# Kernel optimization log

Measured on AMD Instinct MI355X. Metric: run time of the kernel, lower is better.

The kernel has to match this reference:

```python
import jax, jax.numpy as jnp
import numpy as np

B, S, T, V, E, H, D, A = 16, 128, 128, 32000, 512, 512, 512, 512
ENC = 2 * H  # bidirectional encoder output dim
NEG = -1e9


def _w(key, shape, scale=0.05):
    return scale * jax.random.normal(key, shape, dtype=jnp.float32)


def setup_inputs() -> dict:
    key = jax.random.key(0)
    ks = jax.random.split(key, 26)
    src = jax.random.randint(ks[0], (B, S), 1, V)
    tgt = jax.random.randint(ks[1], (B, T), 1, V)
    src_lens = jnp.full((B,), S, dtype=jnp.int32)  # full-length sequences (pack == identity)
    return dict(
        src=src, src_lens=src_lens, tgt=tgt,
        enc_embed=_w(ks[2], (V, E)).at[0].set(0.0),   # padding_idx=0
        Wih_f=_w(ks[3], (4 * H, E)), Whh_f=_w(ks[4], (4 * H, H)),
        bih_f=_w(ks[5], (4 * H,)), bhh_f=_w(ks[6], (4 * H,)),
        Wih_b=_w(ks[7], (4 * H, E)), Whh_b=_w(ks[8], (4 * H, H)),
        bih_b=_w(ks[9], (4 * H,)), bhh_b=_w(ks[10], (4 * H,)),
        Wbh=_w(ks[11], (D, 2 * H)), bbh=_w(ks[12], (D,)),
        Wbc=_w(ks[13], (D, 2 * H)), bbc=_w(ks[14], (D,)),
        Wh_att=_w(ks[15], (A, ENC)), Ws_att=_w(ks[16], (A, D)), v_att=_w(ks[17], (A,)),
        dec_embed=_w(ks[18], (V, E)).at[0].set(0.0),  # padding_idx=0
        Wih_d=_w(ks[19], (4 * D, E + ENC)), Whh_d=_w(ks[20], (4 * D, D)),
        bih_d=_w(ks[21], (4 * D,)), bhh_d=_w(ks[22], (4 * D,)),
        Wfc=_w(ks[23], (V, D + ENC)), bfc=_w(ks[24], (V,)),
    )


def _lstm_cell(x, h, c, Wih, Whh, bih, bhh):
    # PyTorch gate order: i, f, g, o
    g = x @ Wih.T + h @ Whh.T + (bih + bhh)
    i, f, gg, o = jnp.split(g, 4, axis=-1)
    c = jax.nn.sigmoid(f) * c + jax.nn.sigmoid(i) * jnp.tanh(gg)
    h = jax.nn.sigmoid(o) * jnp.tanh(c)
    return h, c


def _run_lstm(xs, Wih, Whh, bih, bhh, hdim):
    # xs: [S, B, E] -> (hs [S, B, hdim], h_last, c_last)
    b = xs.shape[1]
    h0 = jnp.zeros((b, hdim), xs.dtype)

    def step(carry, x):
        h, c = carry
        h, c = _lstm_cell(x, h, c, Wih, Whh, bih, bhh)
        return (h, c), h

    (hT, cT), hs = jax.lax.scan(step, (h0, h0), xs)
    return hs, hT, cT


def reference(src, src_lens, tgt, enc_embed, Wih_f, Whh_f, bih_f, bhh_f,
              Wih_b, Whh_b, bih_b, bhh_b, Wbh, bbh, Wbc, bbc,
              Wh_att, Ws_att, v_att, dec_embed, Wih_d, Whh_d, bih_d, bhh_d,
              Wfc, bfc):
    # ---- BiLSTM encoder (src_lens == S, so packing is the identity) ----
    emb = enc_embed[src]                      # [B, S, E]
    xs = jnp.swapaxes(emb, 0, 1)              # [S, B, E]
    hs_f, hf, _ = _run_lstm(xs, Wih_f, Whh_f, bih_f, bhh_f, H)
    hs_b, hb, _ = _run_lstm(xs[::-1], Wih_b, Whh_b, bih_b, bhh_b, H)
    hs_b = hs_b[::-1]
    enc_out = jnp.swapaxes(jnp.concatenate([hs_f, hs_b], axis=-1), 0, 1)  # [B, S, 2H]

    # ---- bridge (num_layers = 1) ----
    h_cat = jnp.concatenate([hf, hb], axis=-1)  # [B, 2H]
    h0 = jnp.tanh(h_cat @ Wbh.T + bbh)          # [B, D]
    c_cat = jnp.concatenate([hf, hb], axis=-1)
    c0 = jnp.tanh(c_cat @ Wbc.T + bbc)

    mask = jnp.arange(S)[None, :] < src_lens[:, None]  # [B, S]
    enc_proj = jnp.einsum('bse,ae->bsa', enc_out, Wh_att)  # W_h(enc_out), hoisted

    # ---- decoder loop, teacher_forcing = 1.0 ----
    def dec_step(carry, inp_t):
        h, c = carry
        # Bahdanau attention on top-layer hidden state
        score = jnp.einsum('bsa,a->bs', jnp.tanh(enc_proj + (h @ Ws_att.T)[:, None, :]), v_att)
        score = jnp.where(mask, score, NEG)
        attn = jax.nn.softmax(score, axis=-1)
        ctx = jnp.einsum('bs,bse->be', attn, enc_out)       # [B, 2H]
        x = jnp.concatenate([dec_embed[inp_t], ctx], axis=-1)  # [B, E+2H]
        h, c = _lstm_cell(x, h, c, Wih_d, Whh_d, bih_d, bhh_d)
        logits = jnp.concatenate([h, ctx], axis=-1) @ Wfc.T + bfc  # [B, V]
        return (h, c), logits

    inps = tgt[:, :-1].T  # [T-1, B]
    _, logits = jax.lax.scan(dec_step, (h0, c0), inps)
    return jnp.swapaxes(logits, 0, 1)  # [B, T-1, V]
```

## Files before the change

### kernel.cpp

```cpp
#include <hip/hip_runtime.h>

typedef __bf16 bf16x8 __attribute__((ext_vector_type(8)));
typedef float f32x4 __attribute__((ext_vector_type(4)));
typedef unsigned short us;
typedef unsigned long long ull;

#define DEV static __device__ __forceinline__

DEV float bf2f(us u){ union { unsigned u; float f; } x; x.u = ((unsigned)u) << 16; return x.f; }
DEV us f2bf(float f){
  union { float f; unsigned u; } x; x.f = f;
  unsigned r = x.u + 0x7fffu + ((x.u >> 16) & 1u);
  return (us)(r >> 16);
}
DEV unsigned pack2(us lo, us hi){ return (unsigned)lo | ((unsigned)hi << 16); }
DEV float sigm(float x){ return 1.0f / (1.0f + expf(-x)); }
DEV float tanh_fast(float x){ float e = __expf(2.0f * x); return 1.0f - 2.0f / (e + 1.0f); }
DEV void unpk2(unsigned u, float& a, float& b){ a = bf2f((us)u); b = bf2f((us)(u >> 16)); }

DEV unsigned ld4v(const unsigned* p){ return __hip_atomic_load(p, __ATOMIC_RELAXED, __HIP_MEMORY_SCOPE_AGENT); }
DEV ull ld8v(const void* p){ return __hip_atomic_load((const ull*)p, __ATOMIC_RELAXED, __HIP_MEMORY_SCOPE_AGENT); }
DEV void st4v(unsigned* p, unsigned v){ __hip_atomic_store(p, v, __ATOMIC_RELAXED, __HIP_MEMORY_SCOPE_AGENT); }

DEV void gridbar3(unsigned* arr, unsigned ep){
  __syncthreads();
  if (threadIdx.x == 0)
    __hip_atomic_store(arr + (size_t)blockIdx.x * 16, ep, __ATOMIC_RELEASE, __HIP_MEMORY_SCOPE_AGENT);
  if (threadIdx.x < 128){
    while (__hip_atomic_load(arr + (size_t)threadIdx.x * 16, __ATOMIC_RELAXED, __HIP_MEMORY_SCOPE_AGENT) < ep)
      __builtin_amdgcn_s_sleep(4);
  }
  __syncthreads();
}

__global__ void k_f2bf(const float4* __restrict__ in, uint2* __restrict__ out, long n4){
  long stride = (long)gridDim.x * blockDim.x;
  for (long i = (long)blockIdx.x * blockDim.x + threadIdx.x; i < n4; i += stride){
    float4 v = in[i];
    uint2 o; o.x = pack2(f2bf(v.x), f2bf(v.y)); o.y = pack2(f2bf(v.z), f2bf(v.w));
    out[i] = o;
  }
}

__global__ void k_bias3(const float* a0, const float* b0, float* o0,
                        const float* a1, const float* b1, float* o1,
                        const float* a2, const float* b2, float* o2){
  int i = blockIdx.x * 256 + threadIdx.x;
  o0[i] = a0[i] + b0[i];
  o1[i] = a1[i] + b1[i];
  o2[i] = a2[i] + b2[i];
}

__global__ void k_embed(const int* __restrict__ tok, const float* __restrict__ table,
                        us* __restrict__ out){
  int r = blockIdx.x;
  int b = r & 15, pos = r >> 4;
  int idx = tok[b * 128 + pos];
  float4 v = ((const float4*)(table + (size_t)idx * 512))[threadIdx.x];
  uint2 o; o.x = pack2(f2bf(v.x), f2bf(v.y)); o.y = pack2(f2bf(v.z), f2bf(v.w));
  ((uint2*)(out + (size_t)r * 512))[threadIdx.x] = o;
}

template<int MODE>
__global__ __launch_bounds__(256)
void gemm_bt(const us* __restrict__ A, int lda,
             const us* __restrict__ B, int ldb,
             const float* __restrict__ bias,
             void* __restrict__ Cv, int ldc, int K, int mvalid)
{
  __shared__ __align__(16) us As[128 * 64];
  __shared__ __align__(16) us Bs[128 * 64];
  const int tid  = threadIdx.x;
  const int lane = tid & 63, wid = tid >> 6;
  const int wm = (wid >> 1) * 64, wn = (wid & 1) * 64;
  const us* Ab = A + (size_t)blockIdx.y * 128 * lda;
  const us* Bb = B + (size_t)blockIdx.x * 128 * ldb;

  f32x4 acc[4][4] = {};
  bf16x8 ga[4], gb[4];

  #pragma unroll
  for (int r = 0; r < 4; r++){
    int c = tid + r * 256;
    ga[r] = *(const bf16x8*)(Ab + (size_t)(c >> 3) * lda + (c & 7) * 8);
    gb[r] = *(const bf16x8*)(Bb + (size_t)(c >> 3) * ldb + (c & 7) * 8);
  }
  const int nt = K >> 6;
  for (int t = 0; t < nt; t++){
    #pragma unroll
    for (int r = 0; r < 4; r++){
      int c = tid + r * 256;
      int slot = ((c >> 3) * 8 + ((c & 7) ^ ((c >> 3) & 7))) * 8;
      *(bf16x8*)(As + slot) = ga[r];
      *(bf16x8*)(Bs + slot) = gb[r];
    }
    __syncthreads();
    if (t + 1 < nt){
      int k0 = (t + 1) * 64;
      #pragma unroll
      for (int r = 0; r < 4; r++){
        int c = tid + r * 256;
        ga[r] = *(const bf16x8*)(Ab + (size_t)(c >> 3) * lda + k0 + (c & 7) * 8);
        gb[r] = *(const bf16x8*)(Bb + (size_t)(c >> 3) * ldb + k0 + (c & 7) * 8);
      }
    }
    #pragma unroll
    for (int kk = 0; kk < 2; kk++){
      bf16x8 av[4], bv[4];
      #pragma unroll
      for (int i = 0; i < 4; i++){
        int ra = wm + i * 16 + (lane & 15);
        int ua = (kk * 4 + (lane >> 4)) ^ (ra & 7);
        av[i] = *(const bf16x8*)(As + (ra * 8 + ua) * 8);
        int rb = wn + i * 16 + (lane & 15);
        int ub = (kk * 4 + (lane >> 4)) ^ (rb & 7);
        bv[i] = *(const bf16x8*)(Bs + (rb * 8 + ub) * 8);
      }
      #pragma unroll
      for (int i = 0; i < 4; i++)
        #pragma unroll
        for (int j = 0; j < 4; j++)
          acc[i][j] = __builtin_amdgcn_mfma_f32_16x16x32_bf16(av[i], bv[j], acc[i][j], 0, 0, 0);
    }
    if (t + 1 < nt) __syncthreads();
  }

  const int cb = lane & 15, rb4 = (lane >> 4) * 4;
  #pragma unroll
  for (int i = 0; i < 4; i++){
    #pragma unroll
    for (int j = 0; j < 4; j++){
      #pragma unroll
      for (int r = 0; r < 4; r++){
        int row = blockIdx.y * 128 + wm + i * 16 + rb4 + r;
        int col = blockIdx.x * 128 + wn + j * 16 + cb;
        float v = acc[i][j][r];
        if (bias) v += bias[col];
        if (MODE == 0){
          ((float*)Cv)[(size_t)row * ldc + col] = v;
        } else if (MODE == 2){
          ((us*)Cv)[(size_t)row * ldc + col] = f2bf(v);
        } else {
          if (row < mvalid){
            int tt = row >> 4, b = row & 15;
            ((float*)Cv)[((size_t)b * 127 + tt) * 32000 + col] = v;
          }
        }
      }
    }
  }
}

__global__ __launch_bounds__(256)
void enc_persist4(const float* __restrict__ gin_f, const float* __restrict__ gin_b,
                  const us* __restrict__ whhf_bf, const us* __restrict__ whhb_bf,
                  us* __restrict__ enc_out_bf,
                  unsigned* __restrict__ arr)
{
  __shared__ __align__(16) us Wt[2][1024][8];
  __shared__ __align__(16) us Hrow[2][16][520];
  __shared__ __align__(16) f32x4 P[2][4][64];
  __shared__ float gl[2][16][17];
  __shared__ float hvout[2][16][4];

  const int bx = blockIdx.x, tid = threadIdx.x;
  const int lane = tid & 63, wv = tid >> 6;

  for (int d = 0; d < 2; d++){
    const us* srcw = d ? whhb_bf : whhf_bf;
    for (int u = tid; u < 1024; u += 256){
      int ks = u >> 6, ch = (u >> 4) & 3, v = u & 15;
      int n = (v & 3) * 512 + bx * 4 + (v >> 2);
      *(bf16x8*)Wt[d][u] = *(const bf16x8*)(srcw + (size_t)n * 512 + ks * 32 + ch * 8);
    }
  }

  float creg = 0.0f;
  const int cd = (tid >> 6) & 1, cb = tid & 15, cj = (tid >> 4) & 3;

  for (int t = 0; t < 128; t++){
    if (t == 0){
      #pragma unroll
      for (int r = 0; r < 8; r++){
        int u = tid + r * 256;
        int d = u >> 10, b = (u >> 6) & 15, s16 = u & 63;
        *(ull*)&Hrow[d][b][s16 * 8]     = 0ull;
        *(ull*)&Hrow[d][b][s16 * 8 + 4] = 0ull;
      }
    } else {
      #pragma unroll
      for (int r = 0; r < 8; r++){
        int u = tid + r * 256;
        int d = u >> 10, b = (u >> 6) & 15, s16 = u & 63;
        int sp = d ? (128 - t) : (t - 1);
        const us* s = enc_out_bf + ((size_t)b * 128 + sp) * 1024 + d * 512 + s16 * 8;
        ull lo = ld8v(s), hi = ld8v(s + 4);
        *(ull*)&Hrow[d][b][s16 * 8]     = lo;
        *(ull*)&Hrow[d][b][s16 * 8 + 4] = hi;
      }
    }
    __syncthreads();
    #pragma unroll
    for (int d = 0; d < 2; d++){
      f32x4 acc = {};
      #pragma unroll
      for (int m = 0; m < 4; m++){
        int ks = wv * 4 + m;
        int ch = lane >> 4, b = lane & 15;
        acc = __builtin_amdgcn_mfma_f32_16x16x32_bf16(*(const bf16x8*)&Hrow[d][b][ks * 32 + ch * 8],
                                                      *(const bf16x8*)Wt[d][(ks * 4 + ch) * 16 + b],
                                                      acc, 0, 0, 0);
      }
      P[d][wv][lane] = acc;
    }
    __syncthreads();
    if (wv < 2){
      int d = wv;
      f32x4 sum = (P[d][0][lane] + P[d][1][lane]) + (P[d][2][lane] + P[d][3][lane]);
      int v = lane & 15;
      int n = (v & 3) * 512 + bx * 4 + (v >> 2);
      int s_in = d ? (127 - t) : t;
      const float* gg = (d ? gin_b : gin_f) + (size_t)s_in * 16 * 2048 + n;
      #pragma unroll
      for (int r = 0; r < 4; r++){
        int b = (lane >> 4) * 4 + r;
        gl[d][v][b] = sum[r] + gg[(size_t)b * 2048];
      }
    }
    __syncthreads();
    if (tid < 128){
      float ig = sigm (gl[cd][cj * 4 + 0][cb]);
      float fg = sigm (gl[cd][cj * 4 + 1][cb]);
      float g2 = tanhf(gl[cd][cj * 4 + 2][cb]);
      float og = sigm (gl[cd][cj * 4 + 3][cb]);
      float cn = fg * creg + ig * g2;
      float hv = og * tanhf(cn);
      creg = cn;
      hvout[cd][cb][cj] = hv;
    }
    __syncthreads();
    if (tid < 64){
      int d = tid >> 5, rem = tid & 31, b = rem & 15, jp = rem >> 4;
      int s_in = d ? (127 - t) : t;
      st4v((unsigned*)(enc_out_bf + ((size_t)b * 128 + s_in) * 1024 + d * 512 + bx * 4 + jp * 2),
           pack2(f2bf(hvout[d][b][jp * 2]), f2bf(hvout[d][b][jp * 2 + 1])));
    }
    if (t != 127) gridbar3(arr, t + 1);
  }
}

__global__ __launch_bounds__(512)
void k_h0c0(const us* __restrict__ enc_out_bf, const float* __restrict__ Wbh, const float* __restrict__ bbh,
            const float* __restrict__ Wbc, const float* __restrict__ bbc,
            us* __restrict__ h0_bf, float* __restrict__ c_dec)
{
  __shared__ float hc[1024];
  int b = blockIdx.x >> 1, which = blockIdx.x & 1;
  int tid = threadIdx.x;
  hc[tid]       = bf2f(enc_out_bf[((size_t)b * 128 + 127) * 1024 + tid]);
  hc[512 + tid] = bf2f(enc_out_bf[((size_t)b * 128 + 0)   * 1024 + 512 + tid]);
  __syncthreads();
  const float* W = which ? Wbc : Wbh;
  float acc = (which ? bbc : bbh)[tid];
  const float* wr = W + (size_t)tid * 1024;
  for (int k = 0; k < 1024; k += 4){
    float4 w = *(const float4*)(wr + k);
    acc += w.x * hc[k] + w.y * hc[k + 1] + w.z * hc[k + 2] + w.w * hc[k + 3];
  }
  float v = tanhf(acc);
  if (which) c_dec[b * 512 + tid] = v;
  else       h0_bf[b * 512 + tid] = f2bf(v);
}

__global__ __launch_bounds__(256)
void dec_persist6(const us* __restrict__ h0_bf, const float* __restrict__ c_dec0,
                  const float* __restrict__ Ws_att, const float* __restrict__ v_att,
                  const us* __restrict__ enc_proj_bf,
                  const us* __restrict__ enc_out_bf,
                  const int* __restrict__ src_lens,
                  const float* __restrict__ gin_d,
                  const us* __restrict__ whhd_bf, const us* __restrict__ wihd_bf,
                  float* __restrict__ hs_g, float* __restrict__ scores_g,
                  us* __restrict__ hctx,
                  unsigned* __restrict__ arr)
{
  __shared__ __align__(16) us Wh[1024][8];
  __shared__ __align__(16) us Wc[2048][8];
  __shared__ __align__(16) us Ws_r[4][512];
  __shared__ __align__(16) us ep_r[16][512];
  __shared__ __align__(16) us eo_r[128][128];
  __shared__ __align__(16) us Xrow[16][1032];
  __shared__ __align__(16) f32x4 P[4][64];
  __shared__ float g1l[16][17];
  __shared__ float gl[16][17];
  __shared__ float vl[512];
  __shared__ float hsp[4][64];
  __shared__ float hs_b[512];
  __shared__ float att[128];
  __shared__ float cred[2][128];
  __shared__ float sred[8];
  __shared__ float hvs[16][4];

  const int bx = blockIdx.x, tid = threadIdx.x;
  const int lane = tid & 63, wv = tid >> 6;
  const int bB = bx & 15, sQ = bx >> 4;

  for (int u = tid; u < 1024; u += 256){
    int ks = u >> 6, ch = (u >> 4) & 3, v = u & 15;
    int n = (v & 3) * 512 + bx * 4 + (v >> 2);
    *(bf16x8*)Wh[u] = *(const bf16x8*)(whhd_bf + (size_t)n * 512 + ks * 32 + ch * 8);
  }
  for (int u = tid; u < 2048; u += 256){
    int ks = u >> 6, ch = (u >> 4) & 3, v = u & 15;
    int n = (v & 3) * 512 + bx * 4 + (v >> 2);
    *(bf16x8*)Wc[u] = *(const bf16x8*)(wihd_bf + (size_t)n * 1536 + 512 + ks * 32 + ch * 8);
  }
  for (int u = tid; u < 2048; u += 256){
    int a = u >> 9, k = u & 511;
    Ws_r[a][k] = f2bf(Ws_att[(size_t)(bx * 4 + a) * 512 + k]);
  }
  for (int u = tid; u < 1024; u += 256){
    int si = u >> 6, a8 = (u & 63) * 8;
    *(bf16x8*)&ep_r[si][a8] =
      *(const bf16x8*)(enc_proj_bf + ((size_t)bB * 128 + sQ * 16 + si) * 512 + a8);
  }
  for (int u = tid; u < 2048; u += 256){
    int s = u >> 4, k8 = (u & 15) * 8;
    *(bf16x8*)&eo_r[s][k8] =
      *(const bf16x8*)(enc_out_bf + ((size_t)bB * 128 + s) * 1024 + sQ * 128 + k8);
  }
  for (int u = tid; u < 512; u += 256) vl[u] = v_att[u];
  const int slen = src_lens[bB];

  float creg = 0.0f;
  if (tid < 64) creg = c_dec0[(tid & 15) * 512 + bx * 4 + (tid >> 4)];

  for (int t = 0; t < 127; t++){
    const us* hsrc = t ? (hctx + (size_t)(t - 1) * 16 * 1536) : h0_bf;
    const int hstride = t ? 1536 : 512;

    #pragma unroll
    for (int r = 0; r < 4; r++){
      int u = tid + r * 256;
      int b = u >> 6, s16 = u & 63;
      const us* s = hsrc + (size_t)b * hstride + s16 * 8;
      ull lo = ld8v(s), hi = ld8v(s + 4);
      *(ull*)&Xrow[b][s16 * 8]     = lo;
      *(ull*)&Xrow[b][s16 * 8 + 4] = hi;
    }
    __syncthreads();
    {
      f32x4 acc = {};
      #pragma unroll
      for (int m = 0; m < 4; m++){
        int ks = wv * 4 + m;
        int ch = lane >> 4, b = lane & 15;
        acc = __builtin_amdgcn_mfma_f32_16x16x32_bf16(*(const bf16x8*)&Xrow[b][ks * 32 + ch * 8],
                                                      *(const bf16x8*)Wh[(ks * 4 + ch) * 16 + b],
                                                      acc, 0, 0, 0);
      }
      P[wv][lane] = acc;
    }
    {
      int pr = tid & 63, bq = pr & 15, ai = pr >> 4, kq = wv;
      const us* wr = Ws_r[ai] + kq * 128;
      const us* xr = Xrow[bq] + kq * 128;
      float s = 0.f;
      #pragma unroll
      for (int k = 0; k < 128; k += 8){
        bf16x8 xv = *(const bf16x8*)(xr + k);
        bf16x8 wv8 = *(const bf16x8*)(wr + k);
        #pragma unroll
        for (int e = 0; e < 8; e++) s += (float)xv[e] * (float)wv8[e];
      }
      hsp[kq][pr] = s;
    }
    __syncthreads();
    if (wv == 0){
      f32x4 sum = (P[0][lane] + P[1][lane]) + (P[2][lane] + P[3][lane]);
      int v = lane & 15;
      int n = (v & 3) * 512 + bx * 4 + (v >> 2);
      #pragma unroll
      for (int r = 0; r < 4; r++){
        int b = (lane >> 4) * 4 + r;
        g1l[v][b] = sum[r] + gin_d[((size_t)t * 16 + b) * 2048 + n];
      }
    }
    if (tid < 64){
      float v = hsp[0][tid] + hsp[1][tid] + hsp[2][tid] + hsp[3][tid];
      st4v((unsigned*)&hs_g[(tid & 15) * 512 + bx * 4 + (tid >> 4)], __float_as_uint(v));
    }

    gridbar3(arr, 4 * t + 1);

    {
      ull v = ld8v(&hs_g[bB * 512 + tid * 2]);
      *(ull*)&hs_b[tid * 2] = v;
    }
    __syncthreads();
    {
      int si = tid >> 4, part = tid & 15;
      const us* er = ep_r[si] + part * 32;
      const float* hb = hs_b + part * 32;
      const float* vp = vl + part * 32;
      float sv = 0.f;
      #pragma unroll
      for (int a = 0; a < 32; a += 8){
        uint4 u4 = *(const uint4*)(er + a);
        float e0,e1,e2,e3,e4,e5,e6,e7;
        unpk2(u4.x,e0,e1); unpk2(u4.y,e2,e3); unpk2(u4.z,e4,e5); unpk2(u4.w,e6,e7);
        sv += vp[a+0]*tanh_fast(e0+hb[a+0]) + vp[a+1]*tanh_fast(e1+hb[a+1])
            + vp[a+2]*tanh_fast(e2+hb[a+2]) + vp[a+3]*tanh_fast(e3+hb[a+3])
            + vp[a+4]*tanh_fast(e4+hb[a+4]) + vp[a+5]*tanh_fast(e5+hb[a+5])
            + vp[a+6]*tanh_fast(e6+hb[a+6]) + vp[a+7]*tanh_fast(e7+hb[a+7]);
      }
      sv += __shfl_xor(sv, 1);
      sv += __shfl_xor(sv, 2);
      sv += __shfl_xor(sv, 4);
      sv += __shfl_xor(sv, 8);
      if (part == 0){
        int s = sQ * 16 + si;
        st4v((unsigned*)&scores_g[bB * 128 + s], __float_as_uint((s < slen) ? sv : -1e9f));
      }
    }

    gridbar3(arr, 4 * t + 2);

    {
      float x = (tid < 128) ? __uint_as_float(ld4v((unsigned*)&scores_g[bB * 128 + tid])) : -3e38f;
      float m = x;
      #pragma unroll
      for (int o = 32; o; o >>= 1) m = fmaxf(m, __shfl_xor(m, o));
      if (lane == 0) sred[wv] = m;
      __syncthreads();
      m = fmaxf(fmaxf(sred[0], sred[1]), fmaxf(sred[2], sred[3]));
      float e = (tid < 128) ? __expf(x - m) : 0.f;
      float ss = e;
      #pragma unroll
      for (int o = 32; o; o >>= 1) ss += __shfl_xor(ss, o);
      if (lane == 0) sred[4 + wv] = ss;
      __syncthreads();
      float inv = 1.0f / (sred[4] + sred[5] + sred[6] + sred[7]);
      if (tid < 128) att[tid] = e * inv;
    }
    __syncthreads();
    {
      int kk = tid & 127, half = tid >> 7;
      const float* ab = att + half * 64;
      const us* er = &eo_r[half * 64][kk];
      float s = 0.f;
      #pragma unroll 8
      for (int s2 = 0; s2 < 64; s2++)
        s += ab[s2] * bf2f(er[(size_t)s2 * 128]);
      cred[half][kk] = s;
    }
    __syncthreads();
    if (tid < 64){
      int kk2 = tid * 2;
      float c0 = cred[0][kk2]     + cred[1][kk2];
      float c1 = cred[0][kk2 + 1] + cred[1][kk2 + 1];
      st4v((unsigned*)(hctx + ((size_t)t * 16 + bB) * 1536 + 512 + sQ * 128 + kk2),
           pack2(f2bf(c0), f2bf(c1)));
    }

    gridbar3(arr, 4 * t + 3);

    #pragma unroll
    for (int r = 0; r < 8; r++){
      int u = tid + r * 256;
      int b = u >> 7, s16 = u & 127;
      const us* s = hctx + ((size_t)t * 16 + b) * 1536 + 512 + s16 * 8;
      ull lo = ld8v(s), hi = ld8v(s + 4);
      *(ull*)&Xrow[b][s16 * 8]     = lo;
      *(ull*)&Xrow[b][s16 * 8 + 4] = hi;
    }
    __syncthreads();
    {
      f32x4 acc = {};
      #pragma unroll
      for (int m = 0; m < 8; m++){
        int ks = wv * 8 + m;
        int ch = lane >> 4, b = lane & 15;
        acc = __builtin_amdgcn_mfma_f32_16x16x32_bf16(*(const bf16x8*)&Xrow[b][ks * 32 + ch * 8],
                                                      *(const bf16x8*)Wc[(ks * 4 + ch) * 16 + b],
                                                      acc, 0, 0, 0);
      }
      P[wv][lane] = acc;
    }
    __syncthreads();
    if (wv == 0){
      f32x4 sum = (P[0][lane] + P[1][lane]) + (P[2][lane] + P[3][lane]);
      int v = lane & 15;
      #pragma unroll
      for (int r = 0; r < 4; r++){
        int b = (lane >> 4) * 4 + r;
        gl[v][b] = sum[r] + g1l[v][b];
      }
    }
    __syncthreads();
    if (tid < 64){
      int b2 = tid & 15, joff = tid >> 4;
      float ig = sigm (gl[joff * 4 + 0][b2]);
      float fg = sigm (gl[joff * 4 + 1][b2]);
      float g2 = tanhf(gl[joff * 4 + 2][b2]);
      float og = sigm (gl[joff * 4 + 3][b2]);
      float cn = fg * creg + ig * g2;
      float hv = og * tanhf(cn);
      creg = cn;
      hvs[b2][joff] = hv;
    }
    __syncthreads();
    if (tid < 32){
      int b = tid & 15, jp = tid >> 4;
      st4v((unsigned*)(hctx + ((size_t)t * 16 + b) * 1536 + bx * 4 + jp * 2),
           pack2(f2bf(hvs[b][jp * 2]), f2bf(hvs[b][jp * 2 + 1])));
    }
    if (t != 126) gridbar3(arr, 4 * t + 4);
  }
}

extern "C" void kernel_launch(void* const* d_in, const int* in_sizes, int n_in,
                              void* d_out, int out_size, void* d_ws, size_t ws_size,
                              hipStream_t stream)
{
  const int*   src       = (const int*)d_in[0];
  const int*   src_lens  = (const int*)d_in[1];
  const int*   tgt       = (const int*)d_in[2];
  const float* enc_embed = (const float*)d_in[3];
  const float* Wih_f = (const float*)d_in[4];
  const float* Whh_f = (const float*)d_in[5];
  const float* bih_f = (const float*)d_in[6];
  const float* bhh_f = (const float*)d_in[7];
  const float* Wih_b = (const float*)d_in[8];
  const float* Whh_b = (const float*)d_in[9];
  const float* bih_b = (const float*)d_in[10];
  const float* bhh_b = (const float*)d_in[11];
  const float* Wbh = (const float*)d_in[12];
  const float* bbh = (const float*)d_in[13];
  const float* Wbc = (const float*)d_in[14];
  const float* bbc = (const float*)d_in[15];
  const float* Wh_att = (const float*)d_in[16];
  const float* Ws_att = (const float*)d_in[17];
  const float* v_att  = (const float*)d_in[18];
  const float* dec_embed = (const float*)d_in[19];
  const float* Wih_d = (const float*)d_in[20];
  const float* Whh_d = (const float*)d_in[21];
  const float* bih_d = (const float*)d_in[22];
  const float* bhh_d = (const float*)d_in[23];
  const float* Wfc = (const float*)d_in[24];
  const float* bfc = (const float*)d_in[25];
  float* out = (float*)d_out;

  char* base = (char*)d_ws;
  size_t off = 0;
  auto take = [&](size_t bytes) -> char* {
    char* p = base + off;
    off += (bytes + 255) & ~(size_t)255;
    return p;
  };
  us* wfc_bf    = (us*)take((size_t)32000 * 1536 * 2);
  us* emb_e     = (us*)take((size_t)2048 * 512 * 2);
  us* emb_d     = (us*)take((size_t)2048 * 512 * 2);
  us* wihf_bf   = (us*)take((size_t)2048 * 512 * 2);
  us* wihb_bf   = (us*)take((size_t)2048 * 512 * 2);
  us* wihd_bf   = (us*)take((size_t)2048 * 1536 * 2);
  us* whhf_bf   = (us*)take((size_t)2048 * 512 * 2);
  us* whhb_bf   = (us*)take((size_t)2048 * 512 * 2);
  us* whhd_bf   = (us*)take((size_t)2048 * 512 * 2);
  us* whatt_bf  = (us*)take((size_t)512 * 1024 * 2);
  float* gin_f    = (float*)take((size_t)2048 * 2048 * 4);
  float* gin_b    = (float*)take((size_t)2048 * 2048 * 4);
  float* gin_d    = (float*)take((size_t)2048 * 2048 * 4);
  us* enc_out_bf  = (us*)take((size_t)2048 * 1024 * 2);
  us* enc_proj_bf = (us*)take((size_t)2048 * 512 * 2);
  us* hctx        = (us*)take((size_t)2048 * 1536 * 2);
  us* h0_bf       = (us*)take((size_t)16 * 512 * 2);
  float* c_dec    = (float*)take((size_t)16 * 512 * 4);
  float* hs_g     = (float*)take((size_t)16 * 512 * 4);
  float* scores_g = (float*)take((size_t)2048 * 4);
  float* bias_f = (float*)take(2048 * 4);
  float* bias_b = (float*)take(2048 * 4);
  float* bias_d = (float*)take(2048 * 4);
  unsigned* arrE = (unsigned*)take(128 * 16 * 4);
  unsigned* arrD = (unsigned*)take(128 * 16 * 4);

  hipMemsetAsync(emb_d, 0, (size_t)2048 * 512 * 2, stream);
  hipMemsetAsync(hctx, 0, (size_t)2048 * 1536 * 2, stream);
  hipMemsetAsync(arrE, 0, (128 * 16 + 128 * 16) * 4 + 256, stream);

  k_f2bf<<<4096, 256, 0, stream>>>((const float4*)Wfc,   (uint2*)wfc_bf,   (long)32000 * 1536 / 4);
  k_f2bf<<<512,  256, 0, stream>>>((const float4*)Wih_f, (uint2*)wihf_bf,  (long)2048 * 512 / 4);
  k_f2bf<<<512,  256, 0, stream>>>((const float4*)Wih_b, (uint2*)wihb_bf,  (long)2048 * 512 / 4);
  k_f2bf<<<1024, 256, 0, stream>>>((const float4*)Wih_d, (uint2*)wihd_bf,  (long)2048 * 1536 / 4);
  k_f2bf<<<512,  256, 0, stream>>>((const float4*)Whh_f, (uint2*)whhf_bf,  (long)2048 * 512 / 4);
  k_f2bf<<<512,  256, 0, stream>>>((const float4*)Whh_b, (uint2*)whhb_bf,  (long)2048 * 512 / 4);
  k_f2bf<<<512,  256, 0, stream>>>((const float4*)Whh_d, (uint2*)whhd_bf,  (long)2048 * 512 / 4);
  k_f2bf<<<512,  256, 0, stream>>>((const float4*)Wh_att,(uint2*)whatt_bf, (long)512 * 1024 / 4);
  k_bias3<<<8, 256, 0, stream>>>(bih_f, bhh_f, bias_f, bih_b, bhh_b, bias_b, bih_d, bhh_d, bias_d);

  k_embed<<<2048, 128, 0, stream>>>(src, enc_embed, emb_e);
  k_embed<<<2032, 128, 0, stream>>>(tgt, dec_embed, emb_d);

  gemm_bt<0><<<dim3(16, 16), 256, 0, stream>>>(emb_e, 512, wihf_bf, 512,  bias_f, gin_f, 2048, 512, 4096);
  gemm_bt<0><<<dim3(16, 16), 256, 0, stream>>>(emb_e, 512, wihb_bf, 512,  bias_b, gin_b, 2048, 512, 4096);
  gemm_bt<0><<<dim3(16, 16), 256, 0, stream>>>(emb_d, 512, wihd_bf, 1536, bias_d, gin_d, 2048, 512, 4096);

  enc_persist4<<<128, 256, 0, stream>>>(gin_f, gin_b, whhf_bf, whhb_bf, enc_out_bf, arrE);

  k_h0c0<<<32, 512, 0, stream>>>(enc_out_bf, Wbh, bbh, Wbc, bbc, h0_bf, c_dec);

  gemm_bt<2><<<dim3(4, 16), 256, 0, stream>>>(enc_out_bf, 1024, whatt_bf, 1024, nullptr, enc_proj_bf, 512, 1024, 4096);

  dec_persist6<<<128, 256, 0, stream>>>(h0_bf, c_dec, Ws_att, v_att, enc_proj_bf, enc_out_bf, src_lens,
                                        gin_d, whhd_bf, wihd_bf, hs_g, scores_g, hctx, arrD);

  gemm_bt<1><<<dim3(250, 16), 256, 0, stream>>>(hctx, 1536, wfc_bf, 1536, bfc, out, 32000, 1536, 2032);
}
```

Before: 3.821 ms.

## Fuse vocab projection GEMM into persistent decoder and overlap with recurrence

The decoder persistent kernel now launches 256 blocks. Blocks 0-127 run the recurrent decoder. Blocks 128-255 compute the output vocabulary GEMM tile by tile, waiting on a timestep-progress counter so that logits for finished timesteps are produced while the recurrence continues. Separately, the attention softmax drops the max subtraction: scores are exponentiated directly and synchronised with a per-batch 8-block group barrier instead of a full grid barrier, with normalisation folded into the context reduction. This cuts one grid barrier per step but risks overflow for large scores and relies on all 256 blocks being co-resident.

```diff
diff --git a/kernel.cpp b/kernel.cpp
--- a/kernel.cpp
+++ b/kernel.cpp
@@ -29,6 +29,17 @@
   if (threadIdx.x < 128){
     while (__hip_atomic_load(arr + (size_t)threadIdx.x * 16, __ATOMIC_RELAXED, __HIP_MEMORY_SCOPE_AGENT) < ep)
       __builtin_amdgcn_s_sleep(4);
+  }
+  __syncthreads();
+}
+
+DEV void groupbar(unsigned* gbase, int slot, unsigned ep){
+  __syncthreads();
+  if (threadIdx.x == 0)
+    __hip_atomic_store(gbase + slot * 16, ep, __ATOMIC_RELEASE, __HIP_MEMORY_SCOPE_AGENT);
+  if (threadIdx.x < 8){
+    while (__hip_atomic_load(gbase + threadIdx.x * 16, __ATOMIC_RELAXED, __HIP_MEMORY_SCOPE_AGENT) < ep)
+      __builtin_amdgcn_s_sleep(2);
   }
   __syncthreads();
 }
@@ -136,16 +147,8 @@
         int col = blockIdx.x * 128 + wn + j * 16 + cb;
         float v = acc[i][j][r];
         if (bias) v += bias[col];
-        if (MODE == 0){
-          ((float*)Cv)[(size_t)row * ldc + col] = v;
-        } else if (MODE == 2){
-          ((us*)Cv)[(size_t)row * ldc + col] = f2bf(v);
-        } else {
-          if (row < mvalid){
-            int tt = row >> 4, b = row & 15;
-            ((float*)Cv)[((size_t)b * 127 + tt) * 32000 + col] = v;
-          }
-        }
+        if (MODE == 0) ((float*)Cv)[(size_t)row * ldc + col] = v;
+        else           ((us*)Cv)[(size_t)row * ldc + col] = f2bf(v);
       }
     }
   }
@@ -272,38 +275,138 @@
   else       h0_bf[b * 512 + tid] = f2bf(v);
 }
 
+#define SMEM_BYTES 148992
+
 __global__ __launch_bounds__(256)
-void dec_persist6(const us* __restrict__ h0_bf, const float* __restrict__ c_dec0,
-                  const float* __restrict__ Ws_att, const float* __restrict__ v_att,
-                  const us* __restrict__ enc_proj_bf,
-                  const us* __restrict__ enc_out_bf,
-                  const int* __restrict__ src_lens,
-                  const float* __restrict__ gin_d,
-                  const us* __restrict__ whhd_bf, const us* __restrict__ wihd_bf,
-                  float* __restrict__ hs_g, float* __restrict__ scores_g,
-                  us* __restrict__ hctx,
-                  unsigned* __restrict__ arr)
+void dec_fused(const us* __restrict__ h0_bf, const float* __restrict__ c_dec0,
+               const float* __restrict__ Ws_att, const float* __restrict__ v_att,
+               const us* __restrict__ enc_proj_bf, const us* __restrict__ enc_out_bf,
+               const int* __restrict__ src_lens, const float* __restrict__ gin_d,
+               const us* __restrict__ whhd_bf, const us* __restrict__ wihd_bf,
+               float* __restrict__ hs_g, float* __restrict__ esc_g,
+               us* __restrict__ hctx,
+               const us* __restrict__ wfc, const float* __restrict__ bfc,
+               float* __restrict__ out,
+               unsigned* __restrict__ arr, unsigned* __restrict__ arrG,
+               unsigned* __restrict__ tdone)
 {
-  __shared__ __align__(16) us Wh[1024][8];
-  __shared__ __align__(16) us Wc[2048][8];
-  __shared__ __align__(16) us Ws_r[4][512];
-  __shared__ __align__(16) us ep_r[16][512];
-  __shared__ __align__(16) us eo_r[128][128];
-  __shared__ __align__(16) us Xrow[16][1032];
-  __shared__ __align__(16) f32x4 P[4][64];
-  __shared__ float g1l[16][17];
-  __shared__ float gl[16][17];
-  __shared__ float vl[512];
-  __shared__ float hsp[4][64];
-  __shared__ float hs_b[512];
-  __shared__ float att[128];
-  __shared__ float cred[2][128];
-  __shared__ float sred[8];
-  __shared__ float hvs[16][4];
-
-  const int bx = blockIdx.x, tid = threadIdx.x;
+  __shared__ __align__(16) char smem[SMEM_BYTES];
+  const int tid = threadIdx.x;
+
+  if (blockIdx.x >= 128){
+    us* As = (us*)smem;
+    us* Bs = (us*)(smem + 16384);
+    const int lane = tid & 63, wid = tid >> 6;
+    const int wm = (wid >> 1) * 64, wn = (wid & 1) * 64;
+    for (int tile = blockIdx.x - 128; tile < 4000; tile += 128){
+      int rt = tile / 250, ct = tile - rt * 250;
+      unsigned need = (rt == 15) ? 127u : (unsigned)(8 * rt + 8);
+      if (tid == 0){
+        while (ld4v(tdone) < need) __builtin_amdgcn_s_sleep(8);
+      }
+      __syncthreads();
+      const us* Ab = hctx + (size_t)rt * 128 * 1536;
+      const us* Bb = wfc  + (size_t)ct * 128 * 1536;
+      f32x4 acc[4][4] = {};
+      bf16x8 ga[4], gb[4];
+      #pragma unroll
+      for (int r = 0; r < 4; r++){
+        int cc = tid + r * 256;
+        int row = cc >> 3, piece = cc & 7;
+        bool val = (rt * 128 + row) < 2032;
+        union { ull q[2]; bf16x8 v; } u;
+        const us* p = Ab + (size_t)row * 1536 + piece * 8;
+        u.q[0] = val ? ld8v(p) : 0ull;
+        u.q[1] = val ? ld8v(p + 4) : 0ull;
+        ga[r] = u.v;
+        gb[r] = *(const bf16x8*)(Bb + (size_t)row * 1536 + piece * 8);
+      }
+      for (int tk = 0; tk < 24; tk++){
+        #pragma unroll
+        for (int r = 0; r < 4; r++){
+          int cc = tid + r * 256;
+          int slot = ((cc >> 3) * 8 + ((cc & 7) ^ ((cc >> 3) & 7))) * 8;
+          *(bf16x8*)(As + slot) = ga[r];
+          *(bf16x8*)(Bs + slot) = gb[r];
+        }
+        __syncthreads();
+        if (tk + 1 < 24){
+          int k0 = (tk + 1) * 64;
+          #pragma unroll
+          for (int r = 0; r < 4; r++){
+            int cc = tid + r * 256;
+            int row = cc >> 3, piece = cc & 7;
+            bool val = (rt * 128 + row) < 2032;
+            union { ull q[2]; bf16x8 v; } u;
+            const us* p = Ab + (size_t)row * 1536 + k0 + piece * 8;
+            u.q[0] = val ? ld8v(p) : 0ull;
+            u.q[1] = val ? ld8v(p + 4) : 0ull;
+            ga[r] = u.v;
+            gb[r] = *(const bf16x8*)(Bb + (size_t)row * 1536 + k0 + piece * 8);
+          }
+        }
+        #pragma unroll
+        for (int kk = 0; kk < 2; kk++){
+          bf16x8 av[4], bv[4];
+          #pragma unroll
+          for (int i = 0; i < 4; i++){
+            int ra = wm + i * 16 + (lane & 15);
+            int ua = (kk * 4 + (lane >> 4)) ^ (ra & 7);
+            av[i] = *(const bf16x8*)(As + (ra * 8 + ua) * 8);
+            int rb = wn + i * 16 + (lane & 15);
+            int ub = (kk * 4 + (lane >> 4)) ^ (rb & 7);
+            bv[i] = *(const bf16x8*)(Bs + (rb * 8 + ub) * 8);
+          }
+          #pragma unroll
+          for (int i = 0; i < 4; i++)
+            #pragma unroll
+            for (int j = 0; j < 4; j++)
+              acc[i][j] = __builtin_amdgcn_mfma_f32_16x16x32_bf16(av[i], bv[j], acc[i][j], 0, 0, 0);
+        }
+        if (tk + 1 < 24) __syncthreads();
+      }
+      const int cbl = lane & 15, rb4 = (lane >> 4) * 4;
+      #pragma unroll
+      for (int i = 0; i < 4; i++){
+        #pragma unroll
+        for (int j = 0; j < 4; j++){
+          #pragma unroll
+          for (int r = 0; r < 4; r++){
+            int row = rt * 128 + wm + i * 16 + rb4 + r;
+            int col = ct * 128 + wn + j * 16 + cbl;
+            if (row < 2032){
+              float v = acc[i][j][r] + bfc[col];
+              int tt = row >> 4, b = row & 15;
+              out[((size_t)b * 127 + tt) * 32000 + col] = v;
+            }
+          }
+        }
+      }
+    }
+    return;
+  }
+
+  us (*Wh)[8]      = (us(*)[8])(smem);
+  us (*Wc)[8]      = (us(*)[8])(smem + 16384);
+  us (*Ws_r)[512]  = (us(*)[512])(smem + 49152);
+  us (*ep_r)[512]  = (us(*)[512])(smem + 53248);
+  us (*eo_r)[128]  = (us(*)[128])(smem + 69632);
+  us (*Xrow)[1032] = (us(*)[1032])(smem + 102400);
+  f32x4 (*P)[64]   = (f32x4(*)[64])(smem + 135424);
+  float (*g1l)[17] = (float(*)[17])(smem + 139520);
+  float (*gl)[17]  = (float(*)[17])(smem + 140608);
+  float* vl        = (float*)(smem + 141696);
+  float (*hsp)[64] = (float(*)[64])(smem + 143744);
+  float* hs_b      = (float*)(smem + 144768);
+  float* att       = (float*)(smem + 146816);
+  float (*cred)[128] = (float(*)[128])(smem + 147328);
+  float* sred      = (float*)(smem + 148352);
+  float (*hvs)[4]  = (float(*)[4])(smem + 148384);
+
+  const int bx = blockIdx.x;
   const int lane = tid & 63, wv = tid >> 6;
   const int bB = bx & 15, sQ = bx >> 4;
+  unsigned* gbase = arrG + bB * 128;
 
   for (int u = tid; u < 1024; u += 256){
     int ks = u >> 6, ch = (u >> 4) & 3, v = u & 15;
@@ -391,7 +494,7 @@
       st4v((unsigned*)&hs_g[(tid & 15) * 512 + bx * 4 + (tid >> 4)], __float_as_uint(v));
     }
 
-    gridbar3(arr, 4 * t + 1);
+    gridbar3(arr, 3 * t + 1);
 
     {
       ull v = ld8v(&hs_g[bB * 512 + tid * 2]);
@@ -420,28 +523,21 @@
       sv += __shfl_xor(sv, 8);
       if (part == 0){
         int s = sQ * 16 + si;
-        st4v((unsigned*)&scores_g[bB * 128 + s], __float_as_uint((s < slen) ? sv : -1e9f));
-      }
-    }
-
-    gridbar3(arr, 4 * t + 2);
+        float e = (s < slen) ? __expf(sv) : 0.f;
+        st4v((unsigned*)&esc_g[bB * 128 + s], __float_as_uint(e));
+      }
+    }
+
+    groupbar(gbase, sQ, t + 1);
 
     {
-      float x = (tid < 128) ? __uint_as_float(ld4v((unsigned*)&scores_g[bB * 128 + tid])) : -3e38f;
-      float m = x;
-      #pragma unroll
-      for (int o = 32; o; o >>= 1) m = fmaxf(m, __shfl_xor(m, o));
-      if (lane == 0) sred[wv] = m;
-      __syncthreads();
-      m = fmaxf(fmaxf(sred[0], sred[1]), fmaxf(sred[2], sred[3]));
-      float e = (tid < 128) ? __expf(x - m) : 0.f;
+      float e = 0.f;
+      if (tid < 128) e = __uint_as_float(ld4v((unsigned*)&esc_g[bB * 128 + tid]));
+      if (tid < 128) att[tid] = e;
       float ss = e;
       #pragma unroll
       for (int o = 32; o; o >>= 1) ss += __shfl_xor(ss, o);
-      if (lane == 0) sred[4 + wv] = ss;
-      __syncthreads();
-      float inv = 1.0f / (sred[4] + sred[5] + sred[6] + sred[7]);
-      if (tid < 128) att[tid] = e * inv;
+      if (lane == 0) sred[wv] = ss;
     }
     __syncthreads();
     {
@@ -456,14 +552,15 @@
     }
     __syncthreads();
     if (tid < 64){
+      float inv = 1.0f / (sred[0] + sred[1] + sred[2] + sred[3]);
       int kk2 = tid * 2;
-      float c0 = cred[0][kk2]     + cred[1][kk2];
-      float c1 = cred[0][kk2 + 1] + cred[1][kk2 + 1];
+      float c0 = (cred[0][kk2]     + cred[1][kk2])     * inv;
+      float c1 = (cred[0][kk2 + 1] + cred[1][kk2 + 1]) * inv;
       st4v((unsigned*)(hctx + ((size_t)t * 16 + bB) * 1536 + 512 + sQ * 128 + kk2),
            pack2(f2bf(c0), f2bf(c1)));
     }
 
-    gridbar3(arr, 4 * t + 3);
+    gridbar3(arr, 3 * t + 2);
 
     #pragma unroll
     for (int r = 0; r < 8; r++){
@@ -515,7 +612,9 @@
       st4v((unsigned*)(hctx + ((size_t)t * 16 + b) * 1536 + bx * 4 + jp * 2),
            pack2(f2bf(hvs[b][jp * 2]), f2bf(hvs[b][jp * 2 + 1])));
     }
-    if (t != 126) gridbar3(arr, 4 * t + 4);
+    gridbar3(arr, 3 * t + 3);
+    if (bx == 0 && tid == 0)
+      __hip_atomic_store(tdone, (unsigned)(t + 1), __ATOMIC_RELEASE, __HIP_MEMORY_SCOPE_AGENT);
   }
 }
 
@@ -577,16 +676,18 @@
   us* h0_bf       = (us*)take((size_t)16 * 512 * 2);
   float* c_dec    = (float*)take((size_t)16 * 512 * 4);
   float* hs_g     = (float*)take((size_t)16 * 512 * 4);
-  float* scores_g = (float*)take((size_t)2048 * 4);
+  float* esc_g    = (float*)take((size_t)16 * 128 * 4);
   float* bias_f = (float*)take(2048 * 4);
   float* bias_b = (float*)take(2048 * 4);
   float* bias_d = (float*)take(2048 * 4);
-  unsigned* arrE = (unsigned*)take(128 * 16 * 4);
-  unsigned* arrD = (unsigned*)take(128 * 16 * 4);
+  unsigned* arrE  = (unsigned*)take(128 * 16 * 4);
+  unsigned* arrD  = (unsigned*)take(128 * 16 * 4);
+  unsigned* arrG  = (unsigned*)take(16 * 8 * 16 * 4);
+  unsigned* tdone = (unsigned*)take(256);
 
   hipMemsetAsync(emb_d, 0, (size_t)2048 * 512 * 2, stream);
   hipMemsetAsync(hctx, 0, (size_t)2048 * 1536 * 2, stream);
-  hipMemsetAsync(arrE, 0, (128 * 16 + 128 * 16) * 4 + 256, stream);
+  hipMemsetAsync(arrE, 0, (128 * 16 + 128 * 16 + 16 * 8 * 16) * 4 + 256, stream);
 
   k_f2bf<<<4096, 256, 0, stream>>>((const float4*)Wfc,   (uint2*)wfc_bf,   (long)32000 * 1536 / 4);
   k_f2bf<<<512,  256, 0, stream>>>((const float4*)Wih_f, (uint2*)wihf_bf,  (long)2048 * 512 / 4);
@@ -611,8 +712,7 @@
 
   gemm_bt<2><<<dim3(4, 16), 256, 0, stream>>>(enc_out_bf, 1024, whatt_bf, 1024, nullptr, enc_proj_bf, 512, 1024, 4096);
 
-  dec_persist6<<<128, 256, 0, stream>>>(h0_bf, c_dec, Ws_att, v_att, enc_proj_bf, enc_out_bf, src_lens,
-                                        gin_d, whhd_bf, wihd_bf, hs_g, scores_g, hctx, arrD);
-
-  gemm_bt<1><<<dim3(250, 16), 256, 0, stream>>>(hctx, 1536, wfc_bf, 1536, bfc, out, 32000, 1536, 2032);
-}
+  dec_fused<<<256, 256, 0, stream>>>(h0_bf, c_dec, Ws_att, v_att, enc_proj_bf, enc_out_bf, src_lens,
+                                     gin_d, whhd_bf, wihd_bf, hs_g, esc_g, hctx,
+                                     wfc_bf, bfc, out, arrD, arrG, tdone);
+}
```

Result: no change. 3.859 ms (+1.0%).
